# Optimization experiments

Hardware: AMD Instinct MI355X
Metric: run time of the kernel (lower is better)

The kernel has to match this reference:

```python
import jax, jax.numpy as jnp
import numpy as np


def setup_inputs() -> dict:
    key = jax.random.key(0)
    k1, k2, k3 = jax.random.split(key, 3)
    B, S, D = 4, 2048, 1024
    x = jax.random.normal(k1, (B, S, D), dtype=jnp.float32)
    # torch Linear weights: [out_features, in_features]
    w_qkv = jax.random.normal(k2, (3 * D, D), dtype=jnp.float32) * (D ** -0.5)
    w_out = jax.random.normal(k3, (D, D), dtype=jnp.float32) * (D ** -0.5)
    return {"x": x, "w_qkv": w_qkv, "w_out": w_out}


def reference(x, w_qkv, w_out):
    B, S, D = x.shape
    H = 16
    Dh = D // H
    qkv = jnp.einsum("bsd,ed->bse", x, w_qkv)  # [B,S,3D]
    q, k, v = jnp.split(qkv, 3, axis=-1)
    # [B,H,S,Dh]
    q = q.reshape(B, S, H, Dh).transpose(0, 2, 1, 3)
    k = k.reshape(B, S, H, Dh).transpose(0, 2, 1, 3)
    v = v.reshape(B, S, H, Dh).transpose(0, 2, 1, 3)
    scale = 1.0 / jnp.sqrt(jnp.asarray(Dh, dtype=x.dtype))
    scores = jnp.einsum("bhqd,bhkd->bhqk", q, k) * scale
    causal = jnp.tril(jnp.ones((S, S), dtype=bool))
    scores = jnp.where(causal, scores, jnp.finfo(scores.dtype).min)
    attn = jax.nn.softmax(scores, axis=-1)
    out = jnp.einsum("bhqk,bhkd->bhqd", attn, v)
    out = out.transpose(0, 2, 1, 3).reshape(B, S, D)
    return jnp.einsum("bsd,ed->bse", out, w_out)
```

## Files before the change

kernel.cpp:

```cpp
#include <hip/hip_runtime.h>
#include <stdint.h>

typedef __attribute__((ext_vector_type(8))) short short8;
typedef __attribute__((ext_vector_type(4))) float f32x4;
typedef __attribute__((ext_vector_type(16))) float f32x16;
typedef __attribute__((ext_vector_type(4))) unsigned int u32x4;

#define AS1 __attribute__((address_space(1)))
#define AS3 __attribute__((address_space(3)))

#define FSWZ(row) ((((row)) & 7) ^ (((row) >> 3) & 7))

#define KSCL 0.18033688f

__device__ __forceinline__ void gload_lds16(const void* g, void* l) {
  __builtin_amdgcn_global_load_lds((const AS1 void*)g, (AS3 void*)l, 16, 0, 0);
}

__device__ __forceinline__ short f2bf(float f) {
  uint32_t u = __float_as_uint(f);
  u += 0x7fffu + ((u >> 16) & 1u);
  return (short)(u >> 16);
}

__device__ __forceinline__ unsigned int cvtpk(float lo, float hi) {
  unsigned int r;
  asm("v_cvt_pk_bf16_f32 %0, %1, %2" : "=v"(r) : "v"(lo), "v"(hi));
  return r;
}

__device__ __forceinline__ float max3f(float a, float b, float c) {
  return fmaxf(fmaxf(a, b), c);
}

__global__ __launch_bounds__(256) void cvt_all(const float* __restrict__ x,
                                               const float* __restrict__ wq,
                                               const float* __restrict__ wo,
                                               short* __restrict__ xb,
                                               short* __restrict__ wqb,
                                               short* __restrict__ wob) {
  int i = blockIdx.x * 256 + threadIdx.x;
  const float* in;
  short* out;
  if (i < 1048576) {
    in = x + (size_t)i * 8;
    out = xb + (size_t)i * 8;
  } else if (i < 1441792) {
    int j = i - 1048576;
    in = wq + (size_t)j * 8;
    out = wqb + (size_t)j * 8;
  } else {
    int j = i - 1441792;
    in = wo + (size_t)j * 8;
    out = wob + (size_t)j * 8;
  }
  const float4* p = (const float4*)in;
  float4 a = p[0], b = p[1];
  short8 o;
  o[0] = f2bf(a.x); o[1] = f2bf(a.y); o[2] = f2bf(a.z); o[3] = f2bf(a.w);
  o[4] = f2bf(b.x); o[5] = f2bf(b.y); o[6] = f2bf(b.z); o[7] = f2bf(b.w);
  *(short8*)out = o;
}

__global__ __launch_bounds__(256) void gemm_bt(const short* __restrict__ A,
                                               const short* __restrict__ B,
                                               int K, int epi,
                                               short* __restrict__ q,
                                               short* __restrict__ k,
                                               short* __restrict__ v,
                                               float* __restrict__ outF, int N) {
  __shared__ short Sm[16896];
  short* Al = Sm;
  short* Bl = Sm + 8192;
  const int tid = threadIdx.x;
  const int lane = tid & 63;
  const int wv = tid >> 6;
  const int wr = wv >> 1, wc = wv & 1;
  const int gx = gridDim.x;
  const int lin = blockIdx.y * gx + blockIdx.x;
  const int cpx = (gx * gridDim.y) >> 3;
  const int swz = (lin & 7) * cpx + (lin >> 3);
  const int bm = (swz / gx) * 128, bn = (swz % gx) * 128;
  const int l15 = lane & 15, l4 = lane >> 4;

  f32x4 acc[4][4] = {};

  for (int kt = 0; kt < K; kt += 64) {
#pragma unroll
    for (int i = 0; i < 4; ++i) {
      int c = i * 256 + tid;
      int row = c >> 3, col = (c & 7) * 8;
      gload_lds16(A + (size_t)(bm + row) * K + kt + col, (char*)Al + (size_t)c * 16);
      gload_lds16(B + (size_t)(bn + row) * K + kt + col, (char*)Bl + (size_t)c * 16);
    }
    __syncthreads();
#pragma unroll
    for (int ks = 0; ks < 2; ++ks) {
      short8 af[4], bf[4];
#pragma unroll
      for (int mf = 0; mf < 4; ++mf)
        af[mf] = *(const short8*)&Al[(wr * 64 + mf * 16 + l15) * 64 + ks * 32 + l4 * 8];
#pragma unroll
      for (int nf = 0; nf < 4; ++nf)
        bf[nf] = *(const short8*)&Bl[(wc * 64 + nf * 16 + l15) * 64 + ks * 32 + l4 * 8];
#pragma unroll
      for (int mf = 0; mf < 4; ++mf)
#pragma unroll
        for (int nf = 0; nf < 4; ++nf)
          acc[mf][nf] =
              __builtin_amdgcn_mfma_f32_16x16x32_bf16(af[mf], bf[nf], acc[mf][nf], 0, 0, 0);
    }
    __syncthreads();
  }

  if (epi == 0) {
    if (bn >= 2048) {
#pragma unroll
      for (int mf = 0; mf < 4; ++mf)
#pragma unroll
        for (int r = 0; r < 4; ++r) {
          int srow = wr * 64 + mf * 16 + l4 * 4 + r;
#pragma unroll
          for (int nf = 0; nf < 4; ++nf) {
            int dloc = wc * 64 + nf * 16 + l15;
            Sm[dloc * 132 + srow] = f2bf(acc[mf][nf][r]);
          }
        }
      __syncthreads();
      const int bb = bm >> 11, s0 = bm & 2047;
      const int dbase = bn - 2048;
#pragma unroll
      for (int it = 0; it < 8; ++it) {
        int row = it * 16 + (tid >> 4);
        int scol = (tid & 15) * 8;
        short8 val = *(const short8*)&Sm[row * 132 + scol];
        int dglob = dbase + row;
        int hh = dglob >> 6, dh = dglob & 63;
        *(short8*)&v[((size_t)(bb * 16 + hh) * 64 + dh) * 2048 + s0 + scol] = val;
      }
    } else {
#pragma unroll
      for (int mf = 0; mf < 4; ++mf)
#pragma unroll
        for (int r = 0; r < 4; ++r) {
          int m = bm + wr * 64 + mf * 16 + l4 * 4 + r;
          int bb = m >> 11, s = m & 2047;
#pragma unroll
          for (int nf = 0; nf < 4; ++nf) {
            int n = bn + wc * 64 + nf * 16 + l15;
            int which = n >> 10, d = n & 1023, h = d >> 6, dh = d & 63;
            float val = acc[mf][nf][r];
            if (which == 1) val *= KSCL;
            short* dst = (which == 0) ? q : k;
            dst[((size_t)(bb * 16 + h) * 2048 + s) * 64 + dh] = f2bf(val);
          }
        }
    }
  } else {
#pragma unroll
    for (int mf = 0; mf < 4; ++mf)
#pragma unroll
      for (int r = 0; r < 4; ++r) {
        int m = bm + wr * 64 + mf * 16 + l4 * 4 + r;
#pragma unroll
        for (int nf = 0; nf < 4; ++nf) {
          int n = bn + wc * 64 + nf * 16 + l15;
          outF[(size_t)m * N + n] = acc[mf][nf][r];
        }
      }
  }
}

__global__ __launch_bounds__(256) void attn_fwd(const short* __restrict__ Qb,
                                                const short* __restrict__ Kb,
                                                const short* __restrict__ Vtg,
                                                short* __restrict__ Ob) {
  __shared__ short Kl[2][64 * 64];
  __shared__ short Vt[2][64 * 64];
  const int tid = threadIdx.x, lane = tid & 63, wv = tid >> 6;
  const int l31 = lane & 31, l32 = lane >> 5;
  const int bh = blockIdx.x;
  const int qt = (int)gridDim.y - 1 - (int)blockIdx.y;
  const int b = bh >> 4, h = bh & 15;
  const size_t base = (size_t)bh * 2048 * 64;
  const size_t baseV = (size_t)bh * 64 * 2048;
  const int q0 = qt * 128;
  const int qw0 = q0 + wv * 32;
  const int qg = qw0 + l31;

  short8 qf[4];
#pragma unroll
  for (int dk = 0; dk < 4; ++dk)
    qf[dk] = *(const short8*)(Qb + base + (size_t)qg * 64 + dk * 16 + l32 * 8);

  f32x16 oacc[2] = {};
  float mrun = -1e30f, lrun = 0.f;

  const int nt = 2 * qt + 2;
#pragma unroll
  for (int i = 0; i < 2; ++i) {
    int c = i * 256 + tid;
    int row = c >> 3, j = c & 7;
    int js = (j ^ FSWZ(row)) * 8;
    gload_lds16(Kb + base + (size_t)row * 64 + js, (char*)Kl[0] + (size_t)c * 16);
    gload_lds16(Vtg + baseV + (size_t)row * 2048 + js, (char*)Vt[0] + (size_t)c * 16);
  }

  for (int t = 0; t < nt; ++t) {
    const int cur = t & 1;
    const int kv0 = t * 64;
    __syncthreads();

    if (t + 1 < nt) {
      const int kv1 = kv0 + 64;
#pragma unroll
      for (int i = 0; i < 2; ++i) {
        int c = i * 256 + tid;
        int row = c >> 3, j = c & 7;
        int js = (j ^ FSWZ(row)) * 8;
        gload_lds16(Kb + base + (size_t)(kv1 + row) * 64 + js,
                    (char*)Kl[cur ^ 1] + (size_t)c * 16);
        gload_lds16(Vtg + baseV + (size_t)row * 2048 + kv1 + js,
                    (char*)Vt[cur ^ 1] + (size_t)c * 16);
      }
    }

    if (kv0 <= qw0 + 31) {
      f32x16 sc[2] = {};
#pragma unroll
      for (int dk = 0; dk < 4; ++dk)
#pragma unroll
        for (int kb = 0; kb < 2; ++kb) {
          int row = kb * 32 + l31;
          short8 kf =
              *(const short8*)&Kl[cur][row * 64 + (((dk * 2 + l32) ^ FSWZ(row)) * 8)];
          sc[kb] = __builtin_amdgcn_mfma_f32_32x32x16_bf16(kf, qf[dk], sc[kb], 0, 0, 0);
        }

      if (kv0 + 63 > qw0) {
        const int thr2 = qg - kv0 - 4 * l32;
#pragma unroll
        for (int kb = 0; kb < 2; ++kb)
#pragma unroll
          for (int r = 0; r < 16; ++r) {
            if (kb * 32 + ((r & 3) + 8 * (r >> 2)) > thr2) sc[kb][r] = -1e30f;
          }
      }

      float m0 = max3f(sc[0][0], sc[0][1], sc[0][2]);
      float m1 = max3f(sc[0][3], sc[0][4], sc[0][5]);
      float m2 = max3f(sc[0][6], sc[0][7], sc[0][8]);
      float m3 = max3f(sc[0][9], sc[0][10], sc[0][11]);
      float m4 = max3f(sc[0][12], sc[0][13], sc[0][14]);
      float m5 = max3f(sc[0][15], sc[1][0], sc[1][1]);
      float m6 = max3f(sc[1][2], sc[1][3], sc[1][4]);
      float m7 = max3f(sc[1][5], sc[1][6], sc[1][7]);
      float m8 = max3f(sc[1][8], sc[1][9], sc[1][10]);
      float m9 = max3f(sc[1][11], sc[1][12], sc[1][13]);
      float ma = fmaxf(sc[1][14], sc[1][15]);
      float mb = max3f(m0, m1, m2);
      float mc = max3f(m3, m4, m5);
      float md = max3f(m6, m7, m8);
      float me = max3f(m9, ma, mb);
      float mx = max3f(mc, md, me);
      mx = fmaxf(mx, __shfl_xor(mx, 32));
      if (!__all(mx - mrun <= 11.5416f)) {
        float mnew = fmaxf(mrun, mx);
        float alpha = exp2f(mrun - mnew);
        lrun *= alpha;
#pragma unroll
        for (int dt = 0; dt < 2; ++dt)
#pragma unroll
          for (int r = 0; r < 16; ++r) oacc[dt][r] *= alpha;
        mrun = mnew;
      }
      float pp[2][16];
#pragma unroll
      for (int kb = 0; kb < 2; ++kb)
#pragma unroll
        for (int r = 0; r < 16; ++r) pp[kb][r] = exp2f(sc[kb][r] - mrun);
      float s8[8];
#pragma unroll
      for (int i = 0; i < 8; ++i)
        s8[i] = (pp[0][i] + pp[0][i + 8]) + (pp[1][i] + pp[1][i + 8]);
      float ls = ((s8[0] + s8[4]) + (s8[1] + s8[5])) + ((s8[2] + s8[6]) + (s8[3] + s8[7]));
      ls += __shfl_xor(ls, 32);
      lrun += ls;

      unsigned int W[2][4][2];
#pragma unroll
      for (int kb = 0; kb < 2; ++kb)
#pragma unroll
        for (int g = 0; g < 4; ++g)
#pragma unroll
          for (int u = 0; u < 2; ++u)
            W[kb][g][u] = cvtpk(pp[kb][g * 4 + 2 * u], pp[kb][g * 4 + 2 * u + 1]);

      u32x4 pf[4];
#pragma unroll
      for (int kblk = 0; kblk < 4; ++kblk) {
        const int kbh = kblk >> 1;
#pragma unroll
        for (int u = 0; u < 2; ++u) {
          unsigned int A = W[kbh][2 * (kblk & 1)][u];
          unsigned int B = W[kbh][2 * (kblk & 1) + 1][u];
          unsigned int own = l32 ? B : A;
          unsigned int snd = l32 ? A : B;
          unsigned int rcv = (unsigned int)__shfl_xor((int)snd, 32);
          pf[kblk][0 + u] = l32 ? rcv : own;
          pf[kblk][2 + u] = l32 ? own : rcv;
        }
      }

#pragma unroll
      for (int dt = 0; dt < 2; ++dt)
#pragma unroll
        for (int kblk = 0; kblk < 4; ++kblk) {
          int row = dt * 32 + l31;
          short8 vf =
              *(const short8*)&Vt[cur][row * 64 + (((kblk * 2 + l32) ^ FSWZ(row)) * 8)];
          oacc[dt] = __builtin_amdgcn_mfma_f32_32x32x16_bf16(
              vf, __builtin_bit_cast(short8, pf[kblk]), oacc[dt], 0, 0, 0);
        }
    }
  }

  float inv = 1.f / lrun;
#pragma unroll
  for (int dt = 0; dt < 2; ++dt)
#pragma unroll
    for (int r = 0; r < 16; ++r) {
      int d = dt * 32 + (r & 3) + 8 * (r >> 2) + 4 * l32;
      Ob[(size_t)(b * 2048 + qg) * 1024 + h * 64 + d] = f2bf(oacc[dt][r] * inv);
    }
}

extern "C" void kernel_launch(void* const* d_in, const int* in_sizes, int n_in,
                              void* d_out, int out_size, void* d_ws, size_t ws_size,
                              hipStream_t stream) {
  const float* x = (const float*)d_in[0];
  const float* w_qkv = (const float*)d_in[1];
  const float* w_out = (const float*)d_in[2];
  float* out = (float*)d_out;

  char* ws = (char*)d_ws;
  const size_t MB = 1024 * 1024;
  short* xb    = (short*)(ws + 0 * MB);
  short* wqkvb = (short*)(ws + 16 * MB);
  short* woutb = (short*)(ws + 22 * MB);
  short* qb    = (short*)(ws + 24 * MB);
  short* kb    = (short*)(ws + 40 * MB);
  short* vb    = (short*)(ws + 56 * MB);
  short* ao    = xb;

  cvt_all<<<6144, 256, 0, stream>>>(x, w_qkv, w_out, xb, wqkvb, woutb);

  gemm_bt<<<dim3(3072 / 128, 8192 / 128), 256, 0, stream>>>(
      xb, wqkvb, 1024, 0, qb, kb, vb, nullptr, 3072);

  attn_fwd<<<dim3(64, 16), 256, 0, stream>>>(qb, kb, vb, ao);

  gemm_bt<<<dim3(1024 / 128, 8192 / 128), 256, 0, stream>>>(
      ao, woutb, 1024, 1, nullptr, nullptr, nullptr, out, 1024);
}
```

Baseline: 208.7 us.

## Pair complementary causal query tiles per block to balance work and share K/V loads

Each attention block now handles two query tiles, y and 15-y, so every block does roughly the same causal work, and the grid is halved. The K/V tiles loaded into LDS are reused by both query strips, which cuts global K/V traffic for the lower tile. In exchange each block holds two sets of accumulators and Q fragments, so register pressure rises and occupancy may drop. With 512 blocks there are also fewer waves to hide latency.

```diff
diff --git a/kernel.cpp b/kernel.cpp
--- a/kernel.cpp
+++ b/kernel.cpp
@@ -171,6 +171,108 @@
   }
 }
 
+__device__ __forceinline__ void proc_strip(const short* __restrict__ kbuf,
+                                           const short* __restrict__ vbuf,
+                                           const short8 (&qf)[4], int qg, int qw0,
+                                           int kv0, int l31, int l32,
+                                           float& mrun, float& lrun,
+                                           f32x16 (&oacc)[2]) {
+  f32x16 sc[2] = {};
+#pragma unroll
+  for (int dk = 0; dk < 4; ++dk)
+#pragma unroll
+    for (int kb = 0; kb < 2; ++kb) {
+      int row = kb * 32 + l31;
+      short8 kf = *(const short8*)&kbuf[row * 64 + (((dk * 2 + l32) ^ FSWZ(row)) * 8)];
+      sc[kb] = __builtin_amdgcn_mfma_f32_32x32x16_bf16(kf, qf[dk], sc[kb], 0, 0, 0);
+    }
+
+  if (kv0 + 63 > qw0) {
+    const int thr2 = qg - kv0 - 4 * l32;
+#pragma unroll
+    for (int kb = 0; kb < 2; ++kb)
+#pragma unroll
+      for (int r = 0; r < 16; ++r) {
+        if (kb * 32 + ((r & 3) + 8 * (r >> 2)) > thr2) sc[kb][r] = -1e30f;
+      }
+  }
+
+  float m0 = max3f(sc[0][0], sc[0][1], sc[0][2]);
+  float m1 = max3f(sc[0][3], sc[0][4], sc[0][5]);
+  float m2 = max3f(sc[0][6], sc[0][7], sc[0][8]);
+  float m3 = max3f(sc[0][9], sc[0][10], sc[0][11]);
+  float m4 = max3f(sc[0][12], sc[0][13], sc[0][14]);
+  float m5 = max3f(sc[0][15], sc[1][0], sc[1][1]);
+  float m6 = max3f(sc[1][2], sc[1][3], sc[1][4]);
+  float m7 = max3f(sc[1][5], sc[1][6], sc[1][7]);
+  float m8 = max3f(sc[1][8], sc[1][9], sc[1][10]);
+  float m9 = max3f(sc[1][11], sc[1][12], sc[1][13]);
+  float ma = fmaxf(sc[1][14], sc[1][15]);
+  float mb = max3f(m0, m1, m2);
+  float mc = max3f(m3, m4, m5);
+  float md = max3f(m6, m7, m8);
+  float me = max3f(m9, ma, mb);
+  float mx = max3f(mc, md, me);
+  mx = fmaxf(mx, __shfl_xor(mx, 32));
+  if (!__all(mx - mrun <= 11.5416f)) {
+    float mnew = fmaxf(mrun, mx);
+    float alpha = exp2f(mrun - mnew);
+    lrun *= alpha;
+#pragma unroll
+    for (int dt = 0; dt < 2; ++dt)
+#pragma unroll
+      for (int r = 0; r < 16; ++r) oacc[dt][r] *= alpha;
+    mrun = mnew;
+  }
+  float pp[2][16];
+#pragma unroll
+  for (int kb = 0; kb < 2; ++kb)
+#pragma unroll
+    for (int r = 0; r < 16; ++r) pp[kb][r] = exp2f(sc[kb][r] - mrun);
+  float s8[8];
+#pragma unroll
+  for (int i = 0; i < 8; ++i)
+    s8[i] = (pp[0][i] + pp[0][i + 8]) + (pp[1][i] + pp[1][i + 8]);
+  float ls = ((s8[0] + s8[4]) + (s8[1] + s8[5])) + ((s8[2] + s8[6]) + (s8[3] + s8[7]));
+  ls += __shfl_xor(ls, 32);
+  lrun += ls;
+
+  unsigned int W[2][4][2];
+#pragma unroll
+  for (int kb = 0; kb < 2; ++kb)
+#pragma unroll
+    for (int g = 0; g < 4; ++g)
+#pragma unroll
+      for (int u = 0; u < 2; ++u)
+        W[kb][g][u] = cvtpk(pp[kb][g * 4 + 2 * u], pp[kb][g * 4 + 2 * u + 1]);
+
+  u32x4 pf[4];
+#pragma unroll
+  for (int kblk = 0; kblk < 4; ++kblk) {
+    const int kbh = kblk >> 1;
+#pragma unroll
+    for (int u = 0; u < 2; ++u) {
+      unsigned int A = W[kbh][2 * (kblk & 1)][u];
+      unsigned int B = W[kbh][2 * (kblk & 1) + 1][u];
+      unsigned int own = l32 ? B : A;
+      unsigned int snd = l32 ? A : B;
+      unsigned int rcv = (unsigned int)__shfl_xor((int)snd, 32);
+      pf[kblk][0 + u] = l32 ? rcv : own;
+      pf[kblk][2 + u] = l32 ? own : rcv;
+    }
+  }
+
+#pragma unroll
+  for (int dt = 0; dt < 2; ++dt)
+#pragma unroll
+    for (int kblk = 0; kblk < 4; ++kblk) {
+      int row = dt * 32 + l31;
+      short8 vf = *(const short8*)&vbuf[row * 64 + (((kblk * 2 + l32) ^ FSWZ(row)) * 8)];
+      oacc[dt] = __builtin_amdgcn_mfma_f32_32x32x16_bf16(
+          vf, __builtin_bit_cast(short8, pf[kblk]), oacc[dt], 0, 0, 0);
+    }
+}
+
 __global__ __launch_bounds__(256) void attn_fwd(const short* __restrict__ Qb,
                                                 const short* __restrict__ Kb,
                                                 const short* __restrict__ Vtg,
@@ -180,23 +282,26 @@
   const int tid = threadIdx.x, lane = tid & 63, wv = tid >> 6;
   const int l31 = lane & 31, l32 = lane >> 5;
   const int bh = blockIdx.x;
-  const int qt = (int)gridDim.y - 1 - (int)blockIdx.y;
+  const int y = blockIdx.y;
+  const int qtA = y, qtB = 15 - y;
   const int b = bh >> 4, h = bh & 15;
   const size_t base = (size_t)bh * 2048 * 64;
   const size_t baseV = (size_t)bh * 64 * 2048;
-  const int q0 = qt * 128;
-  const int qw0 = q0 + wv * 32;
-  const int qg = qw0 + l31;
-
-  short8 qf[4];
-#pragma unroll
-  for (int dk = 0; dk < 4; ++dk)
-    qf[dk] = *(const short8*)(Qb + base + (size_t)qg * 64 + dk * 16 + l32 * 8);
-
-  f32x16 oacc[2] = {};
-  float mrun = -1e30f, lrun = 0.f;
-
-  const int nt = 2 * qt + 2;
+  const int qw0A = qtA * 128 + wv * 32, qgA = qw0A + l31;
+  const int qw0B = qtB * 128 + wv * 32, qgB = qw0B + l31;
+
+  short8 qfA[4], qfB[4];
+#pragma unroll
+  for (int dk = 0; dk < 4; ++dk) {
+    qfA[dk] = *(const short8*)(Qb + base + (size_t)qgA * 64 + dk * 16 + l32 * 8);
+    qfB[dk] = *(const short8*)(Qb + base + (size_t)qgB * 64 + dk * 16 + l32 * 8);
+  }
+
+  f32x16 oaccA[2] = {}, oaccB[2] = {};
+  float mrunA = -1e30f, lrunA = 0.f;
+  float mrunB = -1e30f, lrunB = 0.f;
+
+  const int nt = 2 * qtB + 2;
 #pragma unroll
   for (int i = 0; i < 2; ++i) {
     int c = i * 256 + tid;
@@ -225,113 +330,21 @@
       }
     }
 
-    if (kv0 <= qw0 + 31) {
-      f32x16 sc[2] = {};
-#pragma unroll
-      for (int dk = 0; dk < 4; ++dk)
-#pragma unroll
-        for (int kb = 0; kb < 2; ++kb) {
-          int row = kb * 32 + l31;
-          short8 kf =
-              *(const short8*)&Kl[cur][row * 64 + (((dk * 2 + l32) ^ FSWZ(row)) * 8)];
-          sc[kb] = __builtin_amdgcn_mfma_f32_32x32x16_bf16(kf, qf[dk], sc[kb], 0, 0, 0);
-        }
-
-      if (kv0 + 63 > qw0) {
-        const int thr2 = qg - kv0 - 4 * l32;
-#pragma unroll
-        for (int kb = 0; kb < 2; ++kb)
-#pragma unroll
-          for (int r = 0; r < 16; ++r) {
-            if (kb * 32 + ((r & 3) + 8 * (r >> 2)) > thr2) sc[kb][r] = -1e30f;
-          }
-      }
-
-      float m0 = max3f(sc[0][0], sc[0][1], sc[0][2]);
-      float m1 = max3f(sc[0][3], sc[0][4], sc[0][5]);
-      float m2 = max3f(sc[0][6], sc[0][7], sc[0][8]);
-      float m3 = max3f(sc[0][9], sc[0][10], sc[0][11]);
-      float m4 = max3f(sc[0][12], sc[0][13], sc[0][14]);
-      float m5 = max3f(sc[0][15], sc[1][0], sc[1][1]);
-      float m6 = max3f(sc[1][2], sc[1][3], sc[1][4]);
-      float m7 = max3f(sc[1][5], sc[1][6], sc[1][7]);
-      float m8 = max3f(sc[1][8], sc[1][9], sc[1][10]);
-      float m9 = max3f(sc[1][11], sc[1][12], sc[1][13]);
-      float ma = fmaxf(sc[1][14], sc[1][15]);
-      float mb = max3f(m0, m1, m2);
-      float mc = max3f(m3, m4, m5);
-      float md = max3f(m6, m7, m8);
-      float me = max3f(m9, ma, mb);
-      float mx = max3f(mc, md, me);
-      mx = fmaxf(mx, __shfl_xor(mx, 32));
-      if (!__all(mx - mrun <= 11.5416f)) {
-        float mnew = fmaxf(mrun, mx);
-        float alpha = exp2f(mrun - mnew);
-        lrun *= alpha;
-#pragma unroll
-        for (int dt = 0; dt < 2; ++dt)
-#pragma unroll
-          for (int r = 0; r < 16; ++r) oacc[dt][r] *= alpha;
-        mrun = mnew;
-      }
-      float pp[2][16];
-#pragma unroll
-      for (int kb = 0; kb < 2; ++kb)
-#pragma unroll
-        for (int r = 0; r < 16; ++r) pp[kb][r] = exp2f(sc[kb][r] - mrun);
-      float s8[8];
-#pragma unroll
-      for (int i = 0; i < 8; ++i)
-        s8[i] = (pp[0][i] + pp[0][i + 8]) + (pp[1][i] + pp[1][i + 8]);
-      float ls = ((s8[0] + s8[4]) + (s8[1] + s8[5])) + ((s8[2] + s8[6]) + (s8[3] + s8[7]));
-      ls += __shfl_xor(ls, 32);
-      lrun += ls;
-
-      unsigned int W[2][4][2];
-#pragma unroll
-      for (int kb = 0; kb < 2; ++kb)
-#pragma unroll
-        for (int g = 0; g < 4; ++g)
-#pragma unroll
-          for (int u = 0; u < 2; ++u)
-            W[kb][g][u] = cvtpk(pp[kb][g * 4 + 2 * u], pp[kb][g * 4 + 2 * u + 1]);
-
-      u32x4 pf[4];
-#pragma unroll
-      for (int kblk = 0; kblk < 4; ++kblk) {
-        const int kbh = kblk >> 1;
-#pragma unroll
-        for (int u = 0; u < 2; ++u) {
-          unsigned int A = W[kbh][2 * (kblk & 1)][u];
-          unsigned int B = W[kbh][2 * (kblk & 1) + 1][u];
-          unsigned int own = l32 ? B : A;
-          unsigned int snd = l32 ? A : B;
-          unsigned int rcv = (unsigned int)__shfl_xor((int)snd, 32);
-          pf[kblk][0 + u] = l32 ? rcv : own;
-          pf[kblk][2 + u] = l32 ? own : rcv;
-        }
-      }
-
-#pragma unroll
-      for (int dt = 0; dt < 2; ++dt)
-#pragma unroll
-        for (int kblk = 0; kblk < 4; ++kblk) {
-          int row = dt * 32 + l31;
-          short8 vf =
-              *(const short8*)&Vt[cur][row * 64 + (((kblk * 2 + l32) ^ FSWZ(row)) * 8)];
-          oacc[dt] = __builtin_amdgcn_mfma_f32_32x32x16_bf16(
-              vf, __builtin_bit_cast(short8, pf[kblk]), oacc[dt], 0, 0, 0);
-        }
-    }
-  }
-
-  float inv = 1.f / lrun;
+    if (kv0 <= qw0A + 31)
+      proc_strip(Kl[cur], Vt[cur], qfA, qgA, qw0A, kv0, l31, l32, mrunA, lrunA, oaccA);
+    if (kv0 <= qw0B + 31)
+      proc_strip(Kl[cur], Vt[cur], qfB, qgB, qw0B, kv0, l31, l32, mrunB, lrunB, oaccB);
+  }
+
+  float invA = 1.f / lrunA;
+  float invB = 1.f / lrunB;
 #pragma unroll
   for (int dt = 0; dt < 2; ++dt)
 #pragma unroll
     for (int r = 0; r < 16; ++r) {
       int d = dt * 32 + (r & 3) + 8 * (r >> 2) + 4 * l32;
-      Ob[(size_t)(b * 2048 + qg) * 1024 + h * 64 + d] = f2bf(oacc[dt][r] * inv);
+      Ob[(size_t)(b * 2048 + qgA) * 1024 + h * 64 + d] = f2bf(oaccA[dt][r] * invA);
+      Ob[(size_t)(b * 2048 + qgB) * 1024 + h * 64 + d] = f2bf(oaccB[dt][r] * invB);
     }
 }
 
@@ -358,7 +371,7 @@
   gemm_bt<<<dim3(3072 / 128, 8192 / 128), 256, 0, stream>>>(
       xb, wqkvb, 1024, 0, qb, kb, vb, nullptr, 3072);
 
-  attn_fwd<<<dim3(64, 16), 256, 0, stream>>>(qb, kb, vb, ao);
+  attn_fwd<<<dim3(64, 8), 256, 0, stream>>>(qb, kb, vb, ao);
 
   gemm_bt<<<dim3(1024 / 128, 8192 / 128), 256, 0, stream>>>(
       ao, woutb, 1024, 1, nullptr, nullptr, nullptr, out, 1024);
```

After: 245.6 us. 17.6% more time.
